# Performance work log

Hardware: AMD Instinct MI355X
Metric: run time of the kernel (lower is better)

The kernel has to match this reference:

```python
import jax, jax.numpy as jnp
import numpy as np

DIM = 768
N_HEAD = 12
HEAD_DIM = 64
INNER = N_HEAD * HEAD_DIM
SCALE = HEAD_DIM ** -0.5


def setup_inputs() -> dict:
    key = jax.random.key(0)
    ks = jax.random.split(key, 12)
    B, Sf, St = 4, 2048, 2048
    from_tensor = jax.random.normal(ks[0], (B, Sf, DIM), dtype=jnp.float32)
    to_tensor = jax.random.normal(ks[1], (B, St, DIM), dtype=jnp.float32)
    attention_mask = jax.random.randint(ks[2], (B, Sf, St), 0, 2, dtype=jnp.int32)
    # Dense layers: kernel ~ RandomNormal (stddev 0.05, keras default), bias zeros
    def kern(k, fan_in, fan_out):
        return 0.05 * jax.random.normal(k, (fan_in, fan_out), dtype=jnp.float32)
    return {
        "from_tensor": from_tensor,
        "to_tensor": to_tensor,
        "attention_mask": attention_mask,
        "Wq": kern(ks[3], DIM, INNER), "bq": jnp.zeros((INNER,), jnp.float32),
        "Wk": kern(ks[4], DIM, INNER), "bk": jnp.zeros((INNER,), jnp.float32),
        "Wv": kern(ks[5], DIM, INNER), "bv": jnp.zeros((INNER,), jnp.float32),
        "Wo": kern(ks[6], INNER, DIM), "bo": jnp.zeros((DIM,), jnp.float32),
    }


def reference(from_tensor, to_tensor, attention_mask, Wq, bq, Wk, bk, Wv, bv, Wo, bo):
    B, Sf, _ = from_tensor.shape
    St = to_tensor.shape[1]
    # projections -> [B, S, n_head, head_dim] -> [B, n_head, S, head_dim]
    def split_heads(x, S):
        return x.reshape(B, S, N_HEAD, HEAD_DIM).transpose(0, 2, 1, 3)
    q = split_heads(from_tensor @ Wq + bq, Sf) * SCALE
    k = split_heads(to_tensor @ Wk + bk, St)
    v = split_heads(to_tensor @ Wv + bv, St)
    # scores [B, H, Sf, St]
    scores = jnp.einsum('bhik,bhjk->bhij', q, k)
    adder = (1.0 - attention_mask.astype(jnp.float32)) * -10000.0
    scores = scores + adder[:, None, :, :]
    probs = jax.nn.softmax(scores, axis=-1)
    out = jnp.einsum('bhij,bhjk->bhik', probs, v)  # [B, H, Sf, Dh]
    out = out.transpose(0, 2, 1, 3).reshape(B, Sf, INNER)
    return out @ Wo + bo
```

## Files before the change

kernel.cpp:

```cpp
#include <hip/hip_runtime.h>
#include <stdint.h>

#define DIM 768
#define NH 12
#define HD 64
#define BSZ 4
#define SEQ 2048
#define MROWS (BSZ*SEQ)

typedef __attribute__((ext_vector_type(8))) short v8s;
typedef __attribute__((ext_vector_type(4))) float v4f;
typedef __attribute__((ext_vector_type(8))) _Float16 v8h;
typedef __attribute__((ext_vector_type(2))) __fp16 v2fp;

__device__ __forceinline__ uint16_t f2bf(float x) {
  union { float f; uint32_t u; } v; v.f = x;
  uint32_t r = v.u + 0x7fffu + ((v.u >> 16) & 1u);
  return (uint16_t)(r >> 16);
}

#if __has_builtin(__builtin_amdgcn_cvt_pk_bf16_f32)
typedef __attribute__((ext_vector_type(2))) __bf16 v2bf;
__device__ __forceinline__ uint32_t pack_bf16(float a, float b) {
  union { v2bf v; uint32_t u; } c;
  c.v = __builtin_amdgcn_cvt_pk_bf16_f32(a, b);
  return c.u;
}
#else
__device__ __forceinline__ uint32_t pack_bf16(float a, float b) {
  return (uint32_t)f2bf(a) | ((uint32_t)f2bf(b) << 16);
}
#endif

__device__ __forceinline__ uint32_t pack_f16(float a, float b) {
#if __has_builtin(__builtin_amdgcn_cvt_pkrtz)
  union { v2fp h; uint32_t u; } c;
  c.h = __builtin_amdgcn_cvt_pkrtz(a, b);
  return c.u;
#else
  union { _Float16 h[2]; uint32_t u; } c;
  c.h[0] = (_Float16)a; c.h[1] = (_Float16)b; return c.u;
#endif
}

__device__ __forceinline__ float fexp2(float x) {
#if __has_builtin(__builtin_amdgcn_exp2f)
  return __builtin_amdgcn_exp2f(x);
#else
  return exp2f(x);
#endif
}

__device__ __forceinline__ void gl16(const void* g, void* l) {
  __builtin_amdgcn_global_load_lds(
      (const __attribute__((address_space(1))) unsigned int*)g,
      (__attribute__((address_space(3))) unsigned int*)l, 16, 0, 0);
}

__global__ void cvt_bf16_kernel(const float* __restrict__ src0, uint16_t* __restrict__ dst0,
                                const float* __restrict__ src1, uint16_t* __restrict__ dst1,
                                int n4) {
  int i = blockIdx.x * blockDim.x + threadIdx.x;
  const float* src = (i < n4) ? src0 : src1;
  uint16_t* dst = (i < n4) ? dst0 : dst1;
  int j = (i < n4) ? i : i - n4;
  float4 v = ((const float4*)src)[j];
  ushort4 o;
  o.x = f2bf(v.x); o.y = f2bf(v.y); o.z = f2bf(v.z); o.w = f2bf(v.w);
  ((ushort4*)dst)[j] = o;
}

__global__ void mask_bits_kernel(const int* __restrict__ src,
                                 unsigned long long* __restrict__ dst, int nwords) {
  int gtid = blockIdx.x * blockDim.x + threadIdx.x;
  int w = gtid >> 6;
  int lane = threadIdx.x & 63;
  if (w >= nwords) return;
  int b  = w >> 16;
  int q  = (w >> 5) & 2047;
  int kt = w & 31;
  int m = src[((size_t)b * SEQ + q) * SEQ + kt * 64 + lane];
  unsigned long long bits = __ballot(m != 0);
  if (lane == 0) dst[((size_t)b * 32 + kt) * SEQ + q] = bits;
}

__global__ void wtrans_kernel(const float* __restrict__ Wq, const float* __restrict__ Wk,
                              const float* __restrict__ Wv, const float* __restrict__ Wo,
                              uint16_t* __restrict__ WT) {
  __shared__ float tile[32][33];
  int z = blockIdx.z;
  const float* src = (z==0) ? Wq : (z==1) ? Wk : (z==2) ? Wv : Wo;
  uint16_t* dst = WT + (size_t)z * DIM * DIM;
  int tx = threadIdx.x, ty = threadIdx.y;
  int x  = blockIdx.x * 32 + tx;
  int y0 = blockIdx.y * 32;
  for (int j = ty; j < 32; j += 8)
    tile[j][tx] = src[(size_t)(y0 + j) * DIM + x];
  __syncthreads();
  int xo = y0 + tx;
  for (int j = ty; j < 32; j += 8)
    dst[(size_t)(blockIdx.x * 32 + j) * DIM + xo] = f2bf(tile[tx][j]);
}

__global__ __launch_bounds__(256) void gemm_kernel(
    const uint16_t* __restrict__ Xf, const uint16_t* __restrict__ Xt,
    const uint16_t* __restrict__ WT, const uint16_t* __restrict__ AO,
    const float* __restrict__ bq, const float* __restrict__ bk,
    const float* __restrict__ bv, const float* __restrict__ bo,
    uint16_t* __restrict__ Qw, uint16_t* __restrict__ Kw, uint16_t* __restrict__ Vw,
    float* __restrict__ Out, int mode_base)
{
  __shared__ alignas(16) uint16_t As[128 * 32];
  __shared__ alignas(16) uint16_t Bs[128 * 32];
  int mode = mode_base + blockIdx.z;
  const uint16_t* A = (mode == 0) ? Xf : (mode == 3 ? AO : Xt);
  const uint16_t* W = WT + (size_t)mode * DIM * DIM;
  const float* bias = (mode == 0) ? bq : (mode == 1) ? bk : (mode == 2) ? bv : bo;

  int m0 = blockIdx.x * 128, n0 = blockIdx.y * 128;
  int tid = threadIdx.x;
  int wave = tid >> 6, lane = tid & 63, lr = lane & 15, quad = lane >> 4;
  int wm = (wave >> 1) * 64, wn = (wave & 1) * 64;

  int seg = (lane & 3) ^ ((lane >> 3) & 3);
  const uint16_t* agl = A + (size_t)(m0 + wave * 32 + (lane >> 2)) * DIM + seg * 8;
  const uint16_t* bgl = W + (size_t)(n0 + wave * 32 + (lane >> 2)) * DIM + seg * 8;
  int lb = wave * 1024;
  int ck = (lr >> 1) & 3;

  v4f acc[4][4];
  v4f vz = {0.f, 0.f, 0.f, 0.f};
  #pragma unroll
  for (int i = 0; i < 4; i++)
    #pragma unroll
    for (int j = 0; j < 4; j++) acc[i][j] = vz;

  for (int k0 = 0; k0 < DIM; k0 += 32) {
    __syncthreads();
    gl16(agl + k0,            &As[lb]);
    gl16(agl + k0 + 16 * DIM, &As[lb + 512]);
    gl16(bgl + k0,            &Bs[lb]);
    gl16(bgl + k0 + 16 * DIM, &Bs[lb + 512]);
    __syncthreads();
    v8s af[4], bfr[4];
    #pragma unroll
    for (int i = 0; i < 4; i++)
      af[i] = *(const v8s*)&As[(wm + i * 16 + lr) * 32 + ((quad ^ ck) << 3)];
    #pragma unroll
    for (int j = 0; j < 4; j++)
      bfr[j] = *(const v8s*)&Bs[(wn + j * 16 + lr) * 32 + ((quad ^ ck) << 3)];
    #pragma unroll
    for (int i = 0; i < 4; i++)
      #pragma unroll
      for (int j = 0; j < 4; j++)
        acc[i][j] = __builtin_amdgcn_mfma_f32_16x16x32_bf16(af[i], bfr[j], acc[i][j], 0, 0, 0);
  }

  float bj[4];
  #pragma unroll
  for (int j = 0; j < 4; j++) bj[j] = bias[n0 + wn + j * 16 + lr];

  if (mode == 3) {
    #pragma unroll
    for (int i = 0; i < 4; i++) {
      int m = m0 + wm + i * 16 + quad * 4;
      #pragma unroll
      for (int j = 0; j < 4; j++) {
        int n = n0 + wn + j * 16 + lr;
        #pragma unroll
        for (int r = 0; r < 4; r++)
          Out[(size_t)(m + r) * DIM + n] = acc[i][j][r] + bj[j];
      }
    }
  } else if (mode == 2) {
    #pragma unroll
    for (int i = 0; i < 4; i++) {
      int m = m0 + wm + i * 16 + quad * 4;
      int b = m >> 11, s0 = m & 2047;
      int kk0 = s0 & 63;
      int pos = (kk0 >> 5) * 32 + ((kk0 >> 2) & 3) * 8 + ((kk0 >> 4) & 1) * 4;
      int chunk = pos >> 3, off = pos & 7;
      #pragma unroll
      for (int j = 0; j < 4; j++) {
        int n = n0 + wn + j * 16 + lr;
        int h = n >> 6, d = n & 63;
        uint2 pk;
        pk.x = pack_f16(acc[i][j][0] + bj[j], acc[i][j][1] + bj[j]);
        pk.y = pack_f16(acc[i][j][2] + bj[j], acc[i][j][3] + bj[j]);
        int idx = (s0 & ~63) + ((chunk ^ (d & 7)) << 3) + off;
        *(uint2*)&Vw[((size_t)(b * NH + h) * HD + d) * SEQ + idx] = pk;
      }
    }
  } else {
    uint16_t* Dst = (mode == 0) ? Qw : Kw;
    float scale = (mode == 0) ? 0.18033688f : 1.0f;
    #pragma unroll
    for (int i = 0; i < 4; i++) {
      int m = m0 + wm + i * 16 + quad * 4;
      int b = m >> 11, s0 = m & 2047;
      #pragma unroll
      for (int j = 0; j < 4; j++) {
        int n = n0 + wn + j * 16 + lr;
        int h = n >> 6, d = n & 63;
        #pragma unroll
        for (int r = 0; r < 4; r++) {
          float v = (acc[i][j][r] + bj[j]) * scale;
          int s = s0 + r;
          int dd = (mode == 1) ? ((((d >> 3) ^ (s & 7)) << 3) + (d & 7)) : d;
          Dst[((size_t)(b * NH + h) * SEQ + s) * HD + dd] = f2bf(v);
        }
      }
    }
  }
}

__global__ __launch_bounds__(256, 6) void flash_kernel(
    const uint16_t* __restrict__ Qg, const uint16_t* __restrict__ Kg,
    const uint16_t* __restrict__ Vg, const unsigned long long* __restrict__ Mb,
    uint16_t* __restrict__ AO)
{
  __shared__ alignas(16) uint16_t Ks[64 * 64];
  __shared__ alignas(16) uint16_t Vs[64 * 64];

  int tid = threadIdx.x, wave = tid >> 6, lane = tid & 63, lr = lane & 15, quad = lane >> 4;
  int bh = blockIdx.y;
  int b = bh / NH, h = bh - b * NH;
  int q0 = blockIdx.x * 64;
  const uint16_t* Qp = Qg + (size_t)bh * SEQ * HD;
  const uint16_t* Kp = Kg + (size_t)bh * SEQ * HD;
  const uint16_t* Vp = Vg + (size_t)bh * HD * SEQ;
  int qg = q0 + wave * 16 + lr;
  const unsigned long long* Mp = Mb + (size_t)b * 32 * SEQ + qg;

  int swk = lr & 7, sh0 = quad * 4;

  v8s qfa = *(const v8s*)&Qp[(size_t)qg * HD + quad * 8];
  v8s qfb = *(const v8s*)&Qp[(size_t)qg * HD + 32 + quad * 8];

  const uint16_t* kgl = Kp + ((size_t)(wave * 16 + (lane >> 3)) * HD + (lane & 7) * 8);
  const uint16_t* vgl = Vp + ((size_t)(wave * 16 + (lane >> 3)) * SEQ + (lane & 7) * 8);
  int lb = wave * 1024;

  v8h ones;
  #pragma unroll
  for (int i = 0; i < 8; i++) ones[i] = (_Float16)1.0f;

  v4f acc[4], lacc;
  v4f vz = {0.f, 0.f, 0.f, 0.f};
  v4f m8 = {-8.f, -8.f, -8.f, -8.f};
  #pragma unroll
  for (int dt = 0; dt < 4; dt++) acc[dt] = vz;
  lacc = vz;

  for (int k0 = 0; k0 < SEQ; k0 += 64) {
    __syncthreads();
    gl16(kgl + (size_t)k0 * HD,       &Ks[lb]);
    gl16(kgl + (size_t)(k0 + 8) * HD, &Ks[lb + 512]);
    gl16(vgl + k0,                    &Vs[lb]);
    gl16(vgl + k0 + (size_t)8 * SEQ,  &Vs[lb + 512]);
    unsigned long long mw = Mp[(size_t)(k0 >> 6) * SEQ];
    __syncthreads();

    uint32_t mlo = (uint32_t)mw, mhi = (uint32_t)(mw >> 32);
    v8h pf[2];
    #pragma unroll
    for (int p = 0; p < 2; p++) {
      v4f sA = m8, sB = m8;
      {
        int rowb = ((2 * p) * 16 + lr) << 6;
        v8s kf0 = *(const v8s*)&Ks[rowb + ((quad ^ swk) << 3)];
        v8s kf1 = *(const v8s*)&Ks[rowb + (((quad + 4) ^ swk) << 3)];
        sA = __builtin_amdgcn_mfma_f32_16x16x32_bf16(kf0, qfa, sA, 0, 0, 0);
        sA = __builtin_amdgcn_mfma_f32_16x16x32_bf16(kf1, qfb, sA, 0, 0, 0);
      }
      {
        int rowb = ((2 * p + 1) * 16 + lr) << 6;
        v8s kf0 = *(const v8s*)&Ks[rowb + ((quad ^ swk) << 3)];
        v8s kf1 = *(const v8s*)&Ks[rowb + (((quad + 4) ^ swk) << 3)];
        sB = __builtin_amdgcn_mfma_f32_16x16x32_bf16(kf0, qfa, sB, 0, 0, 0);
        sB = __builtin_amdgcn_mfma_f32_16x16x32_bf16(kf1, qfb, sB, 0, 0, 0);
      }
      uint32_t mword = p ? mhi : mlo;
      uint32_t b4a = (mword >> sh0) & 15u;
      uint32_t b4b = (mword >> (sh0 + 16)) & 15u;
      float ps[8];
      #pragma unroll
      for (int r = 0; r < 4; r++) {
        ps[r]     = fexp2(sA[r]) * (float)((b4a >> r) & 1u);
        ps[4 + r] = fexp2(sB[r]) * (float)((b4b >> r) & 1u);
      }
      union { uint4 u; v8h h; } cc;
      cc.u.x = pack_f16(ps[0], ps[1]);
      cc.u.y = pack_f16(ps[2], ps[3]);
      cc.u.z = pack_f16(ps[4], ps[5]);
      cc.u.w = pack_f16(ps[6], ps[7]);
      pf[p] = cc.h;
    }

    #pragma unroll
    for (int dt = 0; dt < 4; dt++) {
      int rowb = (dt * 16 + lr) << 6;
      #pragma unroll
      for (int p = 0; p < 2; p++) {
        v8h vv = *(const v8h*)&Vs[rowb + (((p * 4 + quad) ^ swk) << 3)];
        acc[dt] = __builtin_amdgcn_mfma_f32_16x16x32_f16(vv, pf[p], acc[dt], 0, 0, 0);
      }
    }
    lacc = __builtin_amdgcn_mfma_f32_16x16x32_f16(ones, pf[0], lacc, 0, 0, 0);
    lacc = __builtin_amdgcn_mfma_f32_16x16x32_f16(ones, pf[1], lacc, 0, 0, 0);
  }

  float ri = 1.0f / lacc[0];

  #pragma unroll
  for (int dt = 0; dt < 4; dt++) {
    uint2 pk;
    pk.x = pack_bf16(acc[dt][0] * ri, acc[dt][1] * ri);
    pk.y = pack_bf16(acc[dt][2] * ri, acc[dt][3] * ri);
    *(uint2*)&AO[(size_t)(b * SEQ + qg) * DIM + h * HD + dt * 16 + sh0] = pk;
  }
}

extern "C" void kernel_launch(void* const* d_in, const int* in_sizes, int n_in,
                              void* d_out, int out_size, void* d_ws, size_t ws_size,
                              hipStream_t stream) {
  const float* from_t = (const float*)d_in[0];
  const float* to_t   = (const float*)d_in[1];
  const int*   maski  = (const int*)d_in[2];
  const float* Wq = (const float*)d_in[3];  const float* bq = (const float*)d_in[4];
  const float* Wk = (const float*)d_in[5];  const float* bk = (const float*)d_in[6];
  const float* Wv = (const float*)d_in[7];  const float* bv = (const float*)d_in[8];
  const float* Wo = (const float*)d_in[9];  const float* bo = (const float*)d_in[10];

  char* ws = (char*)d_ws;
  size_t off = 0;
  uint16_t* Xf = (uint16_t*)(ws + off); off += (size_t)MROWS * DIM * 2;
  uint16_t* Xt = (uint16_t*)(ws + off); off += (size_t)MROWS * DIM * 2;
  uint16_t* WT = (uint16_t*)(ws + off); off += (size_t)4 * DIM * DIM * 2;
  unsigned long long* Mbits = (unsigned long long*)(ws + off);
  off += (size_t)BSZ * 32 * SEQ * 8;
  uint16_t* Qw = (uint16_t*)(ws + off); off += (size_t)MROWS * DIM * 2;
  uint16_t* Kw = (uint16_t*)(ws + off); off += (size_t)MROWS * DIM * 2;
  uint16_t* Vw = (uint16_t*)(ws + off); off += (size_t)MROWS * DIM * 2;
  uint16_t* AO = (uint16_t*)(ws + off); off += (size_t)MROWS * DIM * 2;
  float* Out = (float*)d_out;

  int nx4 = MROWS * DIM / 4;
  cvt_bf16_kernel<<<2 * nx4 / 256, 256, 0, stream>>>(from_t, Xf, to_t, Xt, nx4);
  int nwords = BSZ * 32 * SEQ;
  mask_bits_kernel<<<nwords * 64 / 256, 256, 0, stream>>>(maski, Mbits, nwords);
  wtrans_kernel<<<dim3(24, 24, 4), dim3(32, 8), 0, stream>>>(Wq, Wk, Wv, Wo, WT);

  gemm_kernel<<<dim3(64, 6, 3), 256, 0, stream>>>(Xf, Xt, WT, AO, bq, bk, bv, bo,
                                                  Qw, Kw, Vw, Out, 0);
  flash_kernel<<<dim3(SEQ / 64, BSZ * NH), 256, 0, stream>>>(Qw, Kw, Vw, Mbits, AO);
  gemm_kernel<<<dim3(64, 6, 1), 256, 0, stream>>>(Xf, Xt, WT, AO, bq, bk, bv, bo,
                                                  Qw, Kw, Vw, Out, 3);
}
```

Before: 327.2 us.

## Double-buffer LDS tiles in GEMM and flash kernels with XCD-aware block remap

Both the projection GEMM and the flash-attention kernel now use two LDS buffers, so the global-to-LDS loads for the next tile are issued before computing on the current one. This replaces the two barriers per iteration with a single wait-and-barrier, hiding global load latency behind MFMA work. The flash kernel also remaps block indices so that consecutive blocks on the same XCD share a batch-head for better L2 reuse, and raises wave priority around its MFMA sections. Doubling LDS use forces the occupancy hint down from 6 to 5 blocks per CU.

```diff
diff --git a/kernel.cpp b/kernel.cpp
--- a/kernel.cpp
+++ b/kernel.cpp
@@ -55,6 +55,12 @@
   __builtin_amdgcn_global_load_lds(
       (const __attribute__((address_space(1))) unsigned int*)g,
       (__attribute__((address_space(3))) unsigned int*)l, 16, 0, 0);
+}
+
+__device__ __forceinline__ void pipe_sync() {
+  asm volatile("s_waitcnt vmcnt(0)" ::: "memory");
+  __builtin_amdgcn_s_barrier();
+  __builtin_amdgcn_sched_barrier(0);
 }
 
 __global__ void cvt_bf16_kernel(const float* __restrict__ src0, uint16_t* __restrict__ dst0,
@@ -110,8 +116,8 @@
     uint16_t* __restrict__ Qw, uint16_t* __restrict__ Kw, uint16_t* __restrict__ Vw,
     float* __restrict__ Out, int mode_base)
 {
-  __shared__ alignas(16) uint16_t As[128 * 32];
-  __shared__ alignas(16) uint16_t Bs[128 * 32];
+  __shared__ alignas(16) uint16_t As[2][128 * 32];
+  __shared__ alignas(16) uint16_t Bs[2][128 * 32];
   int mode = mode_base + blockIdx.z;
   const uint16_t* A = (mode == 0) ? Xf : (mode == 3 ? AO : Xt);
   const uint16_t* W = WT + (size_t)mode * DIM * DIM;
@@ -135,25 +141,36 @@
     #pragma unroll
     for (int j = 0; j < 4; j++) acc[i][j] = vz;
 
-  for (int k0 = 0; k0 < DIM; k0 += 32) {
-    __syncthreads();
-    gl16(agl + k0,            &As[lb]);
-    gl16(agl + k0 + 16 * DIM, &As[lb + 512]);
-    gl16(bgl + k0,            &Bs[lb]);
-    gl16(bgl + k0 + 16 * DIM, &Bs[lb + 512]);
-    __syncthreads();
+  gl16(agl,            &As[0][lb]);
+  gl16(agl + 16 * DIM, &As[0][lb + 512]);
+  gl16(bgl,            &Bs[0][lb]);
+  gl16(bgl + 16 * DIM, &Bs[0][lb + 512]);
+  pipe_sync();
+
+  int cur = 0;
+  const int NT = DIM / 32;
+  for (int t = 0; t < NT; ++t) {
+    if (t + 1 < NT) {
+      int kn = (t + 1) * 32;
+      gl16(agl + kn,            &As[cur ^ 1][lb]);
+      gl16(agl + kn + 16 * DIM, &As[cur ^ 1][lb + 512]);
+      gl16(bgl + kn,            &Bs[cur ^ 1][lb]);
+      gl16(bgl + kn + 16 * DIM, &Bs[cur ^ 1][lb + 512]);
+    }
     v8s af[4], bfr[4];
     #pragma unroll
     for (int i = 0; i < 4; i++)
-      af[i] = *(const v8s*)&As[(wm + i * 16 + lr) * 32 + ((quad ^ ck) << 3)];
+      af[i] = *(const v8s*)&As[cur][(wm + i * 16 + lr) * 32 + ((quad ^ ck) << 3)];
     #pragma unroll
     for (int j = 0; j < 4; j++)
-      bfr[j] = *(const v8s*)&Bs[(wn + j * 16 + lr) * 32 + ((quad ^ ck) << 3)];
+      bfr[j] = *(const v8s*)&Bs[cur][(wn + j * 16 + lr) * 32 + ((quad ^ ck) << 3)];
     #pragma unroll
     for (int i = 0; i < 4; i++)
       #pragma unroll
       for (int j = 0; j < 4; j++)
         acc[i][j] = __builtin_amdgcn_mfma_f32_16x16x32_bf16(af[i], bfr[j], acc[i][j], 0, 0, 0);
+    if (t + 1 < NT) pipe_sync();
+    cur ^= 1;
   }
 
   float bj[4];
@@ -214,18 +231,22 @@
   }
 }
 
-__global__ __launch_bounds__(256, 6) void flash_kernel(
+__global__ __launch_bounds__(256, 5) void flash_kernel(
     const uint16_t* __restrict__ Qg, const uint16_t* __restrict__ Kg,
     const uint16_t* __restrict__ Vg, const unsigned long long* __restrict__ Mb,
     uint16_t* __restrict__ AO)
 {
-  __shared__ alignas(16) uint16_t Ks[64 * 64];
-  __shared__ alignas(16) uint16_t Vs[64 * 64];
+  __shared__ alignas(16) uint16_t Ks[2][64 * 64];
+  __shared__ alignas(16) uint16_t Vs[2][64 * 64];
 
   int tid = threadIdx.x, wave = tid >> 6, lane = tid & 63, lr = lane & 15, quad = lane >> 4;
-  int bh = blockIdx.y;
+
+  int d = blockIdx.x + (blockIdx.y << 5);
+  int nid = (d & 7) * 192 + (d >> 3);
+  int bh = nid >> 5;
+  int q0 = (nid & 31) * 64;
   int b = bh / NH, h = bh - b * NH;
-  int q0 = blockIdx.x * 64;
+
   const uint16_t* Qp = Qg + (size_t)bh * SEQ * HD;
   const uint16_t* Kp = Kg + (size_t)bh * SEQ * HD;
   const uint16_t* Vp = Vg + (size_t)bh * HD * SEQ;
@@ -252,34 +273,47 @@
   for (int dt = 0; dt < 4; dt++) acc[dt] = vz;
   lacc = vz;
 
-  for (int k0 = 0; k0 < SEQ; k0 += 64) {
-    __syncthreads();
-    gl16(kgl + (size_t)k0 * HD,       &Ks[lb]);
-    gl16(kgl + (size_t)(k0 + 8) * HD, &Ks[lb + 512]);
-    gl16(vgl + k0,                    &Vs[lb]);
-    gl16(vgl + k0 + (size_t)8 * SEQ,  &Vs[lb + 512]);
-    unsigned long long mw = Mp[(size_t)(k0 >> 6) * SEQ];
-    __syncthreads();
-
-    uint32_t mlo = (uint32_t)mw, mhi = (uint32_t)(mw >> 32);
+  gl16(kgl,                    &Ks[0][lb]);
+  gl16(kgl + (size_t)8 * HD,   &Ks[0][lb + 512]);
+  gl16(vgl,                    &Vs[0][lb]);
+  gl16(vgl + (size_t)8 * SEQ,  &Vs[0][lb + 512]);
+  unsigned long long mw_cur = Mp[0];
+  pipe_sync();
+
+  int cur = 0;
+  const int NT = SEQ / 64;
+  for (int it = 0; it < NT; ++it) {
+    unsigned long long mw_next = 0;
+    if (it + 1 < NT) {
+      int kn = (it + 1) * 64;
+      gl16(kgl + (size_t)kn * HD,       &Ks[cur ^ 1][lb]);
+      gl16(kgl + (size_t)(kn + 8) * HD, &Ks[cur ^ 1][lb + 512]);
+      gl16(vgl + kn,                    &Vs[cur ^ 1][lb]);
+      gl16(vgl + kn + (size_t)8 * SEQ,  &Vs[cur ^ 1][lb + 512]);
+      mw_next = Mp[(size_t)(it + 1) * SEQ];
+    }
+
+    uint32_t mlo = (uint32_t)mw_cur, mhi = (uint32_t)(mw_cur >> 32);
     v8h pf[2];
     #pragma unroll
     for (int p = 0; p < 2; p++) {
       v4f sA = m8, sB = m8;
+      __builtin_amdgcn_s_setprio(1);
       {
         int rowb = ((2 * p) * 16 + lr) << 6;
-        v8s kf0 = *(const v8s*)&Ks[rowb + ((quad ^ swk) << 3)];
-        v8s kf1 = *(const v8s*)&Ks[rowb + (((quad + 4) ^ swk) << 3)];
+        v8s kf0 = *(const v8s*)&Ks[cur][rowb + ((quad ^ swk) << 3)];
+        v8s kf1 = *(const v8s*)&Ks[cur][rowb + (((quad + 4) ^ swk) << 3)];
         sA = __builtin_amdgcn_mfma_f32_16x16x32_bf16(kf0, qfa, sA, 0, 0, 0);
         sA = __builtin_amdgcn_mfma_f32_16x16x32_bf16(kf1, qfb, sA, 0, 0, 0);
       }
       {
         int rowb = ((2 * p + 1) * 16 + lr) << 6;
-        v8s kf0 = *(const v8s*)&Ks[rowb + ((quad ^ swk) << 3)];
-        v8s kf1 = *(const v8s*)&Ks[rowb + (((quad + 4) ^ swk) << 3)];
+        v8s kf0 = *(const v8s*)&Ks[cur][rowb + ((quad ^ swk) << 3)];
+        v8s kf1 = *(const v8s*)&Ks[cur][rowb + (((quad + 4) ^ swk) << 3)];
         sB = __builtin_amdgcn_mfma_f32_16x16x32_bf16(kf0, qfa, sB, 0, 0, 0);
         sB = __builtin_amdgcn_mfma_f32_16x16x32_bf16(kf1, qfb, sB, 0, 0, 0);
       }
+      __builtin_amdgcn_s_setprio(0);
       uint32_t mword = p ? mhi : mlo;
       uint32_t b4a = (mword >> sh0) & 15u;
       uint32_t b4b = (mword >> (sh0 + 16)) & 15u;
@@ -297,17 +331,23 @@
       pf[p] = cc.h;
     }
 
+    __builtin_amdgcn_s_setprio(1);
     #pragma unroll
     for (int dt = 0; dt < 4; dt++) {
       int rowb = (dt * 16 + lr) << 6;
       #pragma unroll
       for (int p = 0; p < 2; p++) {
-        v8h vv = *(const v8h*)&Vs[rowb + (((p * 4 + quad) ^ swk) << 3)];
+        v8h vv = *(const v8h*)&Vs[cur][rowb + (((p * 4 + quad) ^ swk) << 3)];
         acc[dt] = __builtin_amdgcn_mfma_f32_16x16x32_f16(vv, pf[p], acc[dt], 0, 0, 0);
       }
     }
     lacc = __builtin_amdgcn_mfma_f32_16x16x32_f16(ones, pf[0], lacc, 0, 0, 0);
     lacc = __builtin_amdgcn_mfma_f32_16x16x32_f16(ones, pf[1], lacc, 0, 0, 0);
+    __builtin_amdgcn_s_setprio(0);
+
+    if (it + 1 < NT) pipe_sync();
+    mw_cur = mw_next;
+    cur ^= 1;
   }
 
   float ri = 1.0f / lacc[0];
```

After: 339.2 us. 1.04x slower.
